# Performance work log

Measured on AMD Instinct MI355X. Metric: run time of the kernel, lower is better.

Reference implementation:

```python
import jax, jax.numpy as jnp
import numpy as np

D_MODEL = 2048
N_HEAD = 16
HEAD_DIM = D_MODEL // N_HEAD
FF_MULT = 4
LN_EPS = 1e-5


def layer_norm(x, w, b):
    mu = jnp.mean(x, axis=-1, keepdims=True)
    var = jnp.mean(jnp.square(x - mu), axis=-1, keepdims=True)
    return (x - mu) * jax.lax.rsqrt(var + LN_EPS) * w + b


def setup_inputs() -> dict:
    key = jax.random.key(0)
    ks = jax.random.split(key, 10)
    B, S, D = 2, 2048, D_MODEL
    s = 1.0 / np.sqrt(D)
    inp = {
        "x": jax.random.normal(ks[0], (B, S, D), jnp.float32),
        "token_emb": jax.random.normal(ks[1], (B, S, D), jnp.float32),
        # torch Linear weights are (out_features, in_features)
        "Wq": jax.random.normal(ks[2], (D, D), jnp.float32) * s,
        "Wk": jax.random.normal(ks[3], (D, D), jnp.float32) * s,
        "Wv": jax.random.normal(ks[4], (D, D), jnp.float32) * s,
        "Wo": jax.random.normal(ks[5], (D, D), jnp.float32) * s,
        "W1": jax.random.normal(ks[6], (FF_MULT * D, D), jnp.float32) * s,
        "W2": jax.random.normal(ks[7], (D, FF_MULT * D), jnp.float32) * (1.0 / np.sqrt(FF_MULT * D)),
        "ln1_w": jnp.ones((D,), jnp.float32),
        "ln1_b": jnp.zeros((D,), jnp.float32),
        "ln2_w": jnp.ones((D,), jnp.float32),
        "ln2_b": jnp.zeros((D,), jnp.float32),
    }
    return inp


def reference(x, token_emb, Wq, Wk, Wv, Wo, W1, W2, ln1_w, ln1_b, ln2_w, ln2_b):
    B, S, D = x.shape
    H, Hd = N_HEAD, HEAD_DIM

    h_norm = layer_norm(x, ln1_w, ln1_b)
    # torch Linear: y = x @ W.T
    q = (h_norm @ Wq.T).reshape(B, S, H, Hd).transpose(0, 2, 1, 3)  # (B,H,S,Hd)
    k = (h_norm @ Wk.T).reshape(B, S, H, Hd).transpose(0, 2, 1, 3)
    v = (token_emb @ Wv.T).reshape(B, S, H, Hd).transpose(0, 2, 1, 3)

    scores = jnp.einsum("bhqd,bhkd->bhqk", q, k) / np.sqrt(Hd)
    causal = jnp.tril(jnp.ones((S, S), bool))  # (S,S)
    scores = jnp.where(causal, scores, -jnp.inf)
    weights = jax.nn.softmax(scores, axis=-1)

    attn = jnp.einsum("bhqk,bhkd->bhqd", weights, v)
    attn = attn.transpose(0, 2, 1, 3).reshape(B, S, D)
    attn = attn @ Wo.T
    x = x + attn

    h_ffn = layer_norm(x, ln2_w, ln2_b)
    ffn = jax.nn.gelu(h_ffn @ W1.T, approximate=False) @ W2.T
    return x + ffn
```

## Files before the change

kernel.cpp:

```cpp
#include <hip/hip_runtime.h>
#include <hip/hip_bf16.h>
#include <math.h>

#define D_MODEL 2048
#define SEQ     2048
#define BATCH   2
#define NTOK    (BATCH*SEQ)
#define NHEAD   16
#define HDIM    128
#define FF      8192

typedef float  f32x4  __attribute__((ext_vector_type(4)));
typedef __bf16 bf16x8 __attribute__((ext_vector_type(8)));

__device__ __forceinline__ unsigned short f2bfbits(float f) {
    unsigned u = __builtin_bit_cast(unsigned, f);
    return (unsigned short)((u + 0x7fffu + ((u >> 16) & 1u)) >> 16);
}
__device__ __forceinline__ __bf16 f2bf(float f) {
    unsigned short h = f2bfbits(f);
    return __builtin_bit_cast(__bf16, h);
}

__device__ __forceinline__ void gld_lds16(const void* g, void* l) {
    __builtin_amdgcn_global_load_lds(
        (const __attribute__((address_space(1))) unsigned int*)g,
        (__attribute__((address_space(3))) unsigned int*)l, 16, 0, 0);
}

#define BAR()      __builtin_amdgcn_s_barrier()
#define LGKM(N)    asm volatile("s_waitcnt lgkmcnt(" #N ")" ::: "memory")
#define VMCNT(N)   asm volatile("s_waitcnt vmcnt(" #N ")" ::: "memory")
#define SCHEDB()   __builtin_amdgcn_sched_barrier(0)

__global__ __launch_bounds__(256) void cvt_all(
        const float* __restrict__ tok, const float* __restrict__ wq,
        const float* __restrict__ wk,  const float* __restrict__ wv,
        const float* __restrict__ wo,  const float* __restrict__ w1,
        const float* __restrict__ w2,
        __bf16* __restrict__ tokb, __bf16* __restrict__ wqb,
        __bf16* __restrict__ wkb,  __bf16* __restrict__ wvb,
        __bf16* __restrict__ wob,  __bf16* __restrict__ w1b,
        __bf16* __restrict__ w2b) {
    const size_t M4 = 4u * 1024 * 1024;
    size_t i = (size_t)blockIdx.x * 1024 + (size_t)threadIdx.x * 4;
    const float* src; __bf16* dst; size_t off;
    if      (i < 2*M4)  { src = tok; dst = tokb; off = i; }
    else if (i < 3*M4)  { src = wq;  dst = wqb;  off = i - 2*M4; }
    else if (i < 4*M4)  { src = wk;  dst = wkb;  off = i - 3*M4; }
    else if (i < 5*M4)  { src = wv;  dst = wvb;  off = i - 4*M4; }
    else if (i < 6*M4)  { src = wo;  dst = wob;  off = i - 5*M4; }
    else if (i < 10*M4) { src = w1;  dst = w1b;  off = i - 6*M4; }
    else                { src = w2;  dst = w2b;  off = i - 10*M4; }
    float4 v = *(const float4*)(src + off);
    ushort4 o;
    o.x = f2bfbits(v.x); o.y = f2bfbits(v.y);
    o.z = f2bfbits(v.z); o.w = f2bfbits(v.w);
    *(ushort4*)((unsigned short*)dst + off) = o;
}

__global__ __launch_bounds__(256) void add_reduce(
        const float* __restrict__ p0, const float* __restrict__ p1,
        const float* __restrict__ resid, float* __restrict__ out) {
    int i = blockIdx.x * 256 + threadIdx.x;
    float4 a = ((const float4*)p0)[i];
    float4 b = ((const float4*)p1)[i];
    float4 r = ((const float4*)resid)[i];
    float4 o;
    o.x = a.x + b.x + r.x; o.y = a.y + b.y + r.y;
    o.z = a.z + b.z + r.z; o.w = a.w + b.w + r.w;
    ((float4*)out)[i] = o;
}

__global__ __launch_bounds__(256) void ln_bf16(
        const float* __restrict__ x, const float* __restrict__ w,
        const float* __restrict__ b, __bf16* __restrict__ out) {
    const int row = blockIdx.x;
    const int tid = threadIdx.x;
    const float* xr = x + (size_t)row * D_MODEL;
    float4 v0 = *(const float4*)(xr + tid * 8);
    float4 v1 = *(const float4*)(xr + tid * 8 + 4);
    float va[8] = {v0.x, v0.y, v0.z, v0.w, v1.x, v1.y, v1.z, v1.w};
    float s = 0.f, ss = 0.f;
#pragma unroll
    for (int j = 0; j < 8; ++j) { s += va[j]; ss += va[j] * va[j]; }
#pragma unroll
    for (int m = 32; m; m >>= 1) { s += __shfl_xor(s, m, 64); ss += __shfl_xor(ss, m, 64); }
    __shared__ float red[8];
    const int wid = tid >> 6;
    if ((tid & 63) == 0) { red[wid * 2] = s; red[wid * 2 + 1] = ss; }
    __syncthreads();
    s  = red[0] + red[2] + red[4] + red[6];
    ss = red[1] + red[3] + red[5] + red[7];
    const float mu   = s * (1.0f / D_MODEL);
    const float var  = ss * (1.0f / D_MODEL) - mu * mu;
    const float rstd = rsqrtf(var + 1e-5f);
    const int c = tid * 8;
    ushort4 o0, o1;
    unsigned short ob[8];
#pragma unroll
    for (int j = 0; j < 8; ++j)
        ob[j] = f2bfbits((va[j] - mu) * rstd * w[c + j] + b[c + j]);
    o0.x = ob[0]; o0.y = ob[1]; o0.z = ob[2]; o0.w = ob[3];
    o1.x = ob[4]; o1.y = ob[5]; o1.z = ob[6]; o1.w = ob[7];
    ushort4* op = (ushort4*)(out + (size_t)row * D_MODEL + c);
    op[0] = o0; op[1] = o1;
}


template <int EPI, int MM>
__device__ __forceinline__ void gemm_epi(
        f32x4 (*acc)[4], int BMsz, int WMsz,
        int bm, int bn, int wm, int wn, int lhi, int l16,
        int M, int N, int slice,
        __bf16* __restrict__ Cb, float* __restrict__ Cf,
        const float* __restrict__ resid) {
#pragma unroll
    for (int m = 0; m < MM; ++m) {
        const int row = bm * BMsz + wm * WMsz + m * 16 + lhi * 4;
#pragma unroll
        for (int n = 0; n < 4; ++n) {
            const int col = bn * 256 + wn * 64 + n * 16 + l16;
            if (EPI == 3) {
                const int h = col >> 7, hd = col & 127;
                const size_t obase =
                    ((((size_t)(row >> 11) * NHEAD + h) * HDIM + hd) << 11) + (row & 2047);
                ushort4 o;
                o.x = f2bfbits(acc[m][n][0]); o.y = f2bfbits(acc[m][n][1]);
                o.z = f2bfbits(acc[m][n][2]); o.w = f2bfbits(acc[m][n][3]);
                *(ushort4*)((unsigned short*)Cb + obase) = o;
            } else {
#pragma unroll
                for (int r = 0; r < 4; ++r) {
                    float v = acc[m][n][r];
                    size_t off = (size_t)(row + r) * N + col;
                    if (EPI == 0) {
                        Cb[off] = f2bf(v);
                    } else if (EPI == 1) {
                        Cb[off] = f2bf(0.5f * v * (1.0f + erff(v * 0.70710678118654752f)));
                    } else if (EPI == 2) {
                        Cf[off] = v + resid[off];
                    } else {
                        Cf[(size_t)slice * M * N + off] = v;
                    }
                }
            }
        }
    }
}

template <int EPI, int SPLITK, int GEO>
__device__ __forceinline__ void gemm_core(
        const __bf16* __restrict__ A, const __bf16* __restrict__ Bm,
        __bf16* __restrict__ Cb, float* __restrict__ Cf,
        const float* __restrict__ resid, int M, int N, int K,
        int bm, int bn, int slice, char* smem) {
    const int tid = threadIdx.x;
    const int wid = tid >> 6, lane = tid & 63;
    const int l16 = lane & 15, lhi = lane >> 4;
    const int wm = wid >> 2, wn = wid & 3;
    const int tps = (K >> 6) / SPLITK;
    const int t0 = slice * tps, t1 = t0 + tps;

    const int trow = tid >> 3;
    const int XsT  = ((tid & 7) << 4) ^ ((trow & 7) << 4);
    const int dstT = tid * 16;
    const int maskL = (l16 & 7) << 4;
    const int colK0 = (lhi * 16) ^ maskL;
    const int colK1 = (64 + lhi * 16) ^ maskL;

    if constexpr (GEO == 0) {
        const __bf16* Ag = A  + (size_t)bm * 256 * K;
        const __bf16* Bg = Bm + (size_t)bn * 256 * K;
        const char* sA[4];
        const char* sB[4];
#pragma unroll
        for (int q = 0; q < 4; ++q) {
            sA[q] = (const char*)(Ag + (size_t)(trow + q * 64) * K) + XsT;
            sB[q] = (const char*)(Bg + (size_t)(trow + q * 64) * K) + XsT;
        }
        const int offA = (wm * 128 + l16) * 128;
        const int offB = 32768 + (wn * 64 + l16) * 128;

        f32x4 acc[8][4] = {};
        bf16x8 af0[4][2], af1[4][2], bq0[2][2], bq1[2][2];
        const char *pA0, *pA1, *pB0, *pB1;
        auto ldA = [&](bf16x8 (&dst)[4][2], int qm) {
#pragma unroll
            for (int i = 0; i < 4; ++i) {
                dst[i][0] = *(const bf16x8*)(pA0 + (qm * 4 + i) * 2048);
                dst[i][1] = *(const bf16x8*)(pA1 + (qm * 4 + i) * 2048);
            }
        };
        auto ldB = [&](bf16x8 (&dst)[2][2], int qn) {
#pragma unroll
            for (int j = 0; j < 2; ++j) {
                dst[j][0] = *(const bf16x8*)(pB0 + (qn * 2 + j) * 2048);
                dst[j][1] = *(const bf16x8*)(pB1 + (qn * 2 + j) * 2048);
            }
        };
        auto mfmaQ = [&](bf16x8 (&a)[4][2], bf16x8 (&b)[2][2], int mo, int no) {
#pragma unroll
            for (int i = 0; i < 4; ++i)
#pragma unroll
                for (int j = 0; j < 2; ++j)
#pragma unroll
                    for (int ks = 0; ks < 2; ++ks)
                        acc[mo + i][no + j] = __builtin_amdgcn_mfma_f32_16x16x32_bf16(
                            a[i][ks], b[j][ks], acc[mo + i][no + j], 0, 0, 0);
        };
        auto stageT = [&](int t, int c) {
            char* bA = smem + c * 65536;
            char* bB = bA + 32768;
            const size_t ko = (size_t)t * 128;
#pragma unroll
            for (int q = 0; q < 4; ++q)
                gld_lds16(sA[q] + ko, bA + q * 8192 + dstT);
#pragma unroll
            for (int q = 0; q < 4; ++q)
                gld_lds16(sB[q] + ko, bB + q * 8192 + dstT);
        };

        stageT(t0, 0);
        VMCNT(0);
        BAR();

        for (int t = t0; t < t1; ++t) {
            const int cur = (t - t0) & 1;
            const char* base = smem + cur * 65536;
            pA0 = base + offA + colK0;
            pA1 = base + offA + colK1;
            pB0 = base + offB + colK0;
            pB1 = base + offB + colK1;
            const bool pf = (t + 1 < t1);
            if (pf) stageT(t + 1, cur ^ 1);
            ldA(af0, 0); ldB(bq0, 0);
            __builtin_amdgcn_s_setprio(1);
            mfmaQ(af0, bq0, 0, 0);
            ldB(bq1, 1);
            mfmaQ(af0, bq1, 0, 2);
            ldA(af1, 1);
            mfmaQ(af1, bq0, 4, 0);
            mfmaQ(af1, bq1, 4, 2);
            __builtin_amdgcn_s_setprio(0);
            if (pf) VMCNT(0);
            BAR();
        }
        gemm_epi<EPI, 8>(acc, 256, 128, bm, bn, wm, wn, lhi, l16,
                         M, N, slice, Cb, Cf, resid);
    } else {
        const __bf16* Ag = A  + (size_t)bm * 128 * K;
        const __bf16* Bg = Bm + (size_t)bn * 256 * K;
        const char* sA[2];
        const char* sB[4];
#pragma unroll
        for (int q = 0; q < 2; ++q)
            sA[q] = (const char*)(Ag + (size_t)(trow + q * 64) * K) + XsT;
#pragma unroll
        for (int q = 0; q < 4; ++q)
            sB[q] = (const char*)(Bg + (size_t)(trow + q * 64) * K) + XsT;
        const int offA = (wm * 64 + l16) * 128;
        const int offB = 16384 + (wn * 64 + l16) * 128;

        f32x4 acc[4][4] = {};
        auto stageT = [&](int t, int c) {
            char* base = smem + c * 49152;
            const size_t ko = (size_t)t * 128;
#pragma unroll
            for (int q = 0; q < 2; ++q)
                gld_lds16(sA[q] + ko, base + q * 8192 + dstT);
#pragma unroll
            for (int q = 0; q < 4; ++q)
                gld_lds16(sB[q] + ko, base + 16384 + q * 8192 + dstT);
        };
        stageT(t0, 0);
        if (t0 + 1 < t1) {
            stageT(t0 + 1, 1);
            VMCNT(6);
        } else {
            VMCNT(0);
        }
        BAR();

        for (int t = t0; t < t1; ++t) {
            const int c = (t - t0) % 3;
            if (t + 2 < t1) stageT(t + 2, (c + 2) % 3);
            const char* base = smem + c * 49152;
            const char* pA0 = base + offA + colK0;
            const char* pA1 = base + offA + colK1;
            const char* pB0 = base + offB + colK0;
            const char* pB1 = base + offB + colK1;
            bf16x8 af[4][2], bq[4][2];
#pragma unroll
            for (int i = 0; i < 4; ++i) {
                af[i][0] = *(const bf16x8*)(pA0 + i * 2048);
                af[i][1] = *(const bf16x8*)(pA1 + i * 2048);
            }
#pragma unroll
            for (int j = 0; j < 4; ++j) {
                bq[j][0] = *(const bf16x8*)(pB0 + j * 2048);
                bq[j][1] = *(const bf16x8*)(pB1 + j * 2048);
            }
            __builtin_amdgcn_s_setprio(1);
#pragma unroll
            for (int i = 0; i < 4; ++i)
#pragma unroll
                for (int j = 0; j < 4; ++j)
#pragma unroll
                    for (int ks = 0; ks < 2; ++ks)
                        acc[i][j] = __builtin_amdgcn_mfma_f32_16x16x32_bf16(
                            af[i][ks], bq[j][ks], acc[i][j], 0, 0, 0);
            __builtin_amdgcn_s_setprio(0);
            if (t + 2 < t1) {
                VMCNT(6);
                BAR();
            } else if (t + 1 < t1) {
                VMCNT(0);
                BAR();
            }
        }
        gemm_epi<EPI, 4>(acc, 128, 64, bm, bn, wm, wn, lhi, l16,
                         M, N, slice, Cb, Cf, resid);
    }
}

template <int EPI, int SPLITK, int GEO, int MAP>
__global__ __launch_bounds__(512, 2) void gemm_k(
        const __bf16* __restrict__ A, const __bf16* __restrict__ Bm,
        __bf16* __restrict__ Cb, float* __restrict__ Cf,
        const float* __restrict__ resid, int M, int N, int K) {
    __shared__ __align__(16) char smem[GEO ? 147456 : 131072];
    int bm, bn, slice = 0;
    if (MAP == 0) {
        int id = blockIdx.x;
        const int cpx = gridDim.x >> 3;
        id = (id & 7) * cpx + (id >> 3);
        const int nbn = N >> 8;
        if (SPLITK == 2) {
            const int nblk = (M >> (GEO ? 7 : 8)) * nbn;
            slice = id / nblk;
            id -= slice * nblk;
        }
        bm = id / nbn; bn = id % nbn;
    } else if (MAP == 1) {
        const int x = blockIdx.x & 7, j = blockIdx.x >> 3;
        bn = (x << 2) | (j & 3); bm = j >> 2;
    } else {
        const int x = blockIdx.x & 7, j = blockIdx.x >> 3;
        bm = (x << 2) | (j & 3); bn = j >> 2;
    }
    gemm_core<EPI, SPLITK, GEO>(A, Bm, Cb, Cf, resid, M, N, K, bm, bn, slice, smem);
}

__global__ __launch_bounds__(512, 2) void gemm_qkv(
        const __bf16* __restrict__ hn, const __bf16* __restrict__ wqk,
        __bf16* __restrict__ QKb, const __bf16* __restrict__ tokb,
        const __bf16* __restrict__ wv, __bf16* __restrict__ Vtg) {
    __shared__ __align__(16) char smem[147456];
    const int x = blockIdx.x & 7, j = blockIdx.x >> 3;
    if (j < 32) {
        const int bm = ((x >> 1) << 2) | (j & 3);
        const int bn = ((x & 1) << 3) | (j >> 2);
        gemm_core<0, 1, 0>(hn, wqk, QKb, nullptr, nullptr,
                           NTOK, 2 * D_MODEL, D_MODEL, bm, bn, 0, smem);
    } else {
        const int jv = j - 32;
        const int bm = ((x >> 1) << 3) | (jv & 7);
        const int bn = ((x & 1) << 2) | (jv >> 3);
        gemm_core<3, 1, 1>(tokb, wv, Vtg, nullptr, nullptr,
                           NTOK, D_MODEL, D_MODEL, bm, bn, 0, smem);
    }
}

#define LDQK 4096
__global__ __launch_bounds__(512) void attn_causal(
        const __bf16* __restrict__ Q, const __bf16* __restrict__ K,
        const __bf16* __restrict__ Vt, __bf16* __restrict__ O) {
    const int qt = gridDim.x - 1 - blockIdx.x;
    const int h = blockIdx.y, bb = blockIdx.z;
    const int tid = threadIdx.x, wid = tid >> 6, lane = tid & 63;
    const int l16 = lane & 15, lhi = lane >> 4;
    __shared__ __align__(16) __bf16 Ks[2][64 * 128];
    __shared__ __align__(16) __bf16 Vs[128 * 64];
    __shared__ __align__(16) __bf16 Pl[8][16 * 72];

    const size_t qkbase = ((size_t)bb * SEQ) * LDQK + (size_t)h * HDIM;
    const size_t obase  = ((size_t)bb * SEQ) * D_MODEL + (size_t)h * HDIM;
    const size_t vtbase = (((size_t)bb * NHEAD + h) * HDIM) << 11;
    const int q0 = qt * 128 + wid * 16;

    bf16x8 qf[4];
#pragma unroll
    for (int ks = 0; ks < 4; ++ks)
        qf[ks] = *(const bf16x8*)(Q + qkbase + (size_t)(q0 + l16) * LDQK + ks * 32 + lhi * 8);

    auto stageK = [&](int kt, int buf) {
#pragma unroll
        for (int j = 0; j < 2; ++j) {
            int idx = j * 512 + tid;
            int row = idx >> 4, c8 = idx & 15;
            int c8s = c8 ^ (row & 7);
            gld_lds16(K + qkbase + (size_t)(kt * 64 + row) * LDQK + c8s * 8,
                      &Ks[buf][0] + idx * 8);
        }
    };
    auto stageV = [&](int kt) {
#pragma unroll
        for (int j = 0; j < 2; ++j) {
            int idx = j * 512 + tid;
            int row = idx >> 3, c8 = idx & 7;
            int c8s = c8 ^ (row & 7);
            gld_lds16(Vt + vtbase + (size_t)row * SEQ + kt * 64 + c8s * 8, Vs + idx * 8);
        }
    };

    f32x4 accO[8] = {};
    float m_run[4], l_run[4];
#pragma unroll
    for (int r = 0; r < 4; ++r) { m_run[r] = -1e30f; l_run[r] = 0.f; }

    const float scale2 = 0.08838834764831845f * 1.4426950408889634f;
    const int NKT = (qt + 1) * 2;

    stageK(0, 0);
    VMCNT(0);
    BAR();
    SCHEDB();

    for (int kt = 0; kt < NKT; ++kt) {
        const int cb = kt & 1;
        const bool pf = (kt + 1 < NKT);
        stageV(kt);
        if (pf) stageK(kt + 1, cb ^ 1);

        f32x4 s[4] = {};
        __builtin_amdgcn_s_setprio(1);
#pragma unroll
        for (int nb = 0; nb < 4; ++nb) {
            const int tok = nb * 16 + l16;
#pragma unroll
            for (int ks = 0; ks < 4; ++ks) {
                int co = (ks * 64 + lhi * 16) ^ ((tok & 7) << 4);
                bf16x8 kf = *(const bf16x8*)((const char*)&Ks[cb][0] + tok * 256 + co);
                s[nb] = __builtin_amdgcn_mfma_f32_16x16x32_bf16(qf[ks], kf, s[nb], 0, 0, 0);
            }
        }
        __builtin_amdgcn_s_setprio(0);

        if (((kt + 1) << 6) > q0) {
#pragma unroll
            for (int nb = 0; nb < 4; ++nb)
#pragma unroll
                for (int r = 0; r < 4; ++r) {
                    float sv = s[nb][r] * scale2;
                    if ((kt * 64 + nb * 16 + l16) > (q0 + lhi * 4 + r)) sv = -1e30f;
                    s[nb][r] = sv;
                }
        } else {
#pragma unroll
            for (int nb = 0; nb < 4; ++nb)
#pragma unroll
                for (int r = 0; r < 4; ++r) s[nb][r] *= scale2;
        }

        float alpha[4];
#pragma unroll
        for (int r = 0; r < 4; ++r) {
            float mx = fmaxf(fmaxf(s[0][r], s[1][r]), fmaxf(s[2][r], s[3][r]));
#pragma unroll
            for (int m = 8; m; m >>= 1) mx = fmaxf(mx, __shfl_xor(mx, m, 64));
            float mnew = fmaxf(m_run[r], mx);
            alpha[r] = exp2f(m_run[r] - mnew);
            float rs = 0.f;
#pragma unroll
            for (int nb = 0; nb < 4; ++nb) {
                float p = exp2f(s[nb][r] - mnew);
                s[nb][r] = p;
                rs += p;
            }
#pragma unroll
            for (int m = 8; m; m >>= 1) rs += __shfl_xor(rs, m, 64);
            l_run[r] = l_run[r] * alpha[r] + rs;
            m_run[r] = mnew;
        }
#pragma unroll
        for (int d8 = 0; d8 < 8; ++d8)
#pragma unroll
            for (int r = 0; r < 4; ++r) accO[d8][r] *= alpha[r];
#pragma unroll
        for (int nb = 0; nb < 4; ++nb)
#pragma unroll
            for (int r = 0; r < 4; ++r)
                Pl[wid][(lhi * 4 + r) * 72 + nb * 16 + l16] = f2bf(s[nb][r]);

        if (pf) { VMCNT(2); } else { VMCNT(0); }
        BAR();
        SCHEDB();

        __builtin_amdgcn_s_setprio(1);
#pragma unroll
        for (int ks2 = 0; ks2 < 2; ++ks2) {
            bf16x8 pa = *(const bf16x8*)(&Pl[wid][l16 * 72 + ks2 * 32 + lhi * 8]);
#pragma unroll
            for (int d8 = 0; d8 < 8; ++d8) {
                const int d = d8 * 16 + l16;
                const int co = ((ks2 * 4 + lhi) ^ (d & 7)) << 4;
                bf16x8 vf = *(const bf16x8*)((const char*)Vs + d * 128 + co);
                accO[d8] = __builtin_amdgcn_mfma_f32_16x16x32_bf16(pa, vf, accO[d8], 0, 0, 0);
            }
        }
        __builtin_amdgcn_s_setprio(0);

        VMCNT(0);
        BAR();
        SCHEDB();
    }

#pragma unroll
    for (int d8 = 0; d8 < 8; ++d8)
#pragma unroll
        for (int r = 0; r < 4; ++r) {
            float o = accO[d8][r] / l_run[r];
            O[obase + (size_t)(q0 + lhi * 4 + r) * D_MODEL + d8 * 16 + l16] = f2bf(o);
        }
}

extern "C" void kernel_launch(void* const* d_in, const int* in_sizes, int n_in,
                              void* d_out, int out_size, void* d_ws, size_t ws_size,
                              hipStream_t stream) {
    const float* x    = (const float*)d_in[0];
    const float* tok  = (const float*)d_in[1];
    const float* Wq   = (const float*)d_in[2];
    const float* Wk   = (const float*)d_in[3];
    const float* Wv   = (const float*)d_in[4];
    const float* Wo   = (const float*)d_in[5];
    const float* W1   = (const float*)d_in[6];
    const float* W2   = (const float*)d_in[7];
    const float* ln1w = (const float*)d_in[8];
    const float* ln1b = (const float*)d_in[9];
    const float* ln2w = (const float*)d_in[10];
    const float* ln2b = (const float*)d_in[11];
    float* out = (float*)d_out;

    char* ws = (char*)d_ws;
    size_t off = 0;
    auto alloc = [&](size_t bytes) { void* p = ws + off; off += bytes; return p; };
    __bf16* tokb  = (__bf16*)alloc((size_t)NTOK * D_MODEL * 2);
    __bf16* hnorm = (__bf16*)alloc((size_t)NTOK * D_MODEL * 2);
    __bf16* wqb   = (__bf16*)alloc((size_t)D_MODEL * D_MODEL * 2);
    __bf16* wkb   = (__bf16*)alloc((size_t)D_MODEL * D_MODEL * 2);
    __bf16* wvb   = (__bf16*)alloc((size_t)D_MODEL * D_MODEL * 2);
    __bf16* wob   = (__bf16*)alloc((size_t)D_MODEL * D_MODEL * 2);
    __bf16* w1b   = (__bf16*)alloc((size_t)FF * D_MODEL * 2);
    __bf16* w2b   = (__bf16*)alloc((size_t)D_MODEL * FF * 2);
    __bf16* QKb   = (__bf16*)alloc((size_t)NTOK * 2 * D_MODEL * 2);
    __bf16* Vtg   = (__bf16*)alloc((size_t)NTOK * D_MODEL * 2);
    __bf16* Ab    = (__bf16*)alloc((size_t)NTOK * D_MODEL * 2);
    float*  x2    = (float*)alloc((size_t)NTOK * D_MODEL * 4);
    __bf16* gb    = QKb;
    float*  p0    = (float*)(ws);
    float*  p1    = p0 + (size_t)NTOK * D_MODEL;

    cvt_all<<<56 * 1024, 256, 0, stream>>>(tok, Wq, Wk, Wv, Wo, W1, W2,
                                           tokb, wqb, wkb, wvb, wob, w1b, w2b);

    ln_bf16<<<NTOK, 256, 0, stream>>>(x, ln1w, ln1b, hnorm);

    gemm_qkv<<<512, 512, 0, stream>>>(hnorm, wqb, QKb, tokb, wvb, Vtg);

    attn_causal<<<dim3(SEQ / 128, NHEAD, BATCH), 512, 0, stream>>>(QKb, QKb + D_MODEL, Vtg, Ab);

    gemm_k<2, 1, 1, 2><<<256, 512, 0, stream>>>(Ab, wob, nullptr, x2, x,
                                                NTOK, D_MODEL, D_MODEL);

    ln_bf16<<<NTOK, 256, 0, stream>>>(x2, ln2w, ln2b, hnorm);

    gemm_k<1, 1, 0, 1><<<512, 512, 0, stream>>>(hnorm, w1b, gb, nullptr, nullptr,
                                                NTOK, FF, D_MODEL);
    gemm_k<4, 2, 0, 0><<<256, 512, 0, stream>>>(gb, w2b, nullptr, p0, nullptr,
                                                NTOK, D_MODEL, FF);
    add_reduce<<<(NTOK * D_MODEL) / 1024, 256, 0, stream>>>(p0, p1, x2, out);
}
```

Before: 633.3 us.

## Fuse LN1 into conversion kernel, lazy softmax rescale, fold residual into split-K

Merges the first layernorm into the weight and activation bf16 conversion kernel, removing one launch. In attention, the online softmax skips the rescale of the running max and accumulator when the row max grows by at most 8 (log2 units), avoiding exp and multiply work on most tiles. The split-K FFN2 GEMM now writes slice 0 plus the residual straight to the output and slice 1 to a scratch buffer, so the final reduce reads two arrays instead of three. The lazy rescale adds a wave-wide vote and a branch, and lets probabilities reach up to 2^8 before bf16 conversion.

New measurement: 686.8 us. 8.4% more time.

```diff
diff --git a/kernel.cpp b/kernel.cpp
--- a/kernel.cpp
+++ b/kernel.cpp
@@ -33,7 +33,9 @@
 #define VMCNT(N)   asm volatile("s_waitcnt vmcnt(" #N ")" ::: "memory")
 #define SCHEDB()   __builtin_amdgcn_sched_barrier(0)
 
-__global__ __launch_bounds__(256) void cvt_all(
+__global__ __launch_bounds__(256) void prep(
+        const float* __restrict__ x, const float* __restrict__ ln1w,
+        const float* __restrict__ ln1b, __bf16* __restrict__ hnorm,
         const float* __restrict__ tok, const float* __restrict__ wq,
         const float* __restrict__ wk,  const float* __restrict__ wv,
         const float* __restrict__ wo,  const float* __restrict__ w1,
@@ -42,34 +44,63 @@
         __bf16* __restrict__ wkb,  __bf16* __restrict__ wvb,
         __bf16* __restrict__ wob,  __bf16* __restrict__ w1b,
         __bf16* __restrict__ w2b) {
-    const size_t M4 = 4u * 1024 * 1024;
-    size_t i = (size_t)blockIdx.x * 1024 + (size_t)threadIdx.x * 4;
-    const float* src; __bf16* dst; size_t off;
-    if      (i < 2*M4)  { src = tok; dst = tokb; off = i; }
-    else if (i < 3*M4)  { src = wq;  dst = wqb;  off = i - 2*M4; }
-    else if (i < 4*M4)  { src = wk;  dst = wkb;  off = i - 3*M4; }
-    else if (i < 5*M4)  { src = wv;  dst = wvb;  off = i - 4*M4; }
-    else if (i < 6*M4)  { src = wo;  dst = wob;  off = i - 5*M4; }
-    else if (i < 10*M4) { src = w1;  dst = w1b;  off = i - 6*M4; }
-    else                { src = w2;  dst = w2b;  off = i - 10*M4; }
-    float4 v = *(const float4*)(src + off);
-    ushort4 o;
-    o.x = f2bfbits(v.x); o.y = f2bfbits(v.y);
-    o.z = f2bfbits(v.z); o.w = f2bfbits(v.w);
-    *(ushort4*)((unsigned short*)dst + off) = o;
-}
-
-__global__ __launch_bounds__(256) void add_reduce(
-        const float* __restrict__ p0, const float* __restrict__ p1,
-        const float* __restrict__ resid, float* __restrict__ out) {
+    const int tid = threadIdx.x;
+    if (blockIdx.x < NTOK) {
+        const int row = blockIdx.x;
+        const float* xr = x + (size_t)row * D_MODEL;
+        float4 v0 = *(const float4*)(xr + tid * 8);
+        float4 v1 = *(const float4*)(xr + tid * 8 + 4);
+        float va[8] = {v0.x, v0.y, v0.z, v0.w, v1.x, v1.y, v1.z, v1.w};
+        float s = 0.f, ss = 0.f;
+#pragma unroll
+        for (int j = 0; j < 8; ++j) { s += va[j]; ss += va[j] * va[j]; }
+#pragma unroll
+        for (int m = 32; m; m >>= 1) { s += __shfl_xor(s, m, 64); ss += __shfl_xor(ss, m, 64); }
+        __shared__ float red[8];
+        const int wid = tid >> 6;
+        if ((tid & 63) == 0) { red[wid * 2] = s; red[wid * 2 + 1] = ss; }
+        __syncthreads();
+        s  = red[0] + red[2] + red[4] + red[6];
+        ss = red[1] + red[3] + red[5] + red[7];
+        const float mu   = s * (1.0f / D_MODEL);
+        const float var  = ss * (1.0f / D_MODEL) - mu * mu;
+        const float rstd = rsqrtf(var + 1e-5f);
+        const int c = tid * 8;
+        ushort4 o0, o1;
+        unsigned short ob[8];
+#pragma unroll
+        for (int j = 0; j < 8; ++j)
+            ob[j] = f2bfbits((va[j] - mu) * rstd * ln1w[c + j] + ln1b[c + j]);
+        o0.x = ob[0]; o0.y = ob[1]; o0.z = ob[2]; o0.w = ob[3];
+        o1.x = ob[4]; o1.y = ob[5]; o1.z = ob[6]; o1.w = ob[7];
+        ushort4* op = (ushort4*)(hnorm + (size_t)row * D_MODEL + c);
+        op[0] = o0; op[1] = o1;
+    } else {
+        const size_t M4 = 4u * 1024 * 1024;
+        size_t i = (size_t)(blockIdx.x - NTOK) * 1024 + (size_t)tid * 4;
+        const float* src; __bf16* dst; size_t off;
+        if      (i < 2*M4)  { src = tok; dst = tokb; off = i; }
+        else if (i < 3*M4)  { src = wq;  dst = wqb;  off = i - 2*M4; }
+        else if (i < 4*M4)  { src = wk;  dst = wkb;  off = i - 3*M4; }
+        else if (i < 5*M4)  { src = wv;  dst = wvb;  off = i - 4*M4; }
+        else if (i < 6*M4)  { src = wo;  dst = wob;  off = i - 5*M4; }
+        else if (i < 10*M4) { src = w1;  dst = w1b;  off = i - 6*M4; }
+        else                { src = w2;  dst = w2b;  off = i - 10*M4; }
+        float4 v = *(const float4*)(src + off);
+        ushort4 o;
+        o.x = f2bfbits(v.x); o.y = f2bfbits(v.y);
+        o.z = f2bfbits(v.z); o.w = f2bfbits(v.w);
+        *(ushort4*)((unsigned short*)dst + off) = o;
+    }
+}
+
+__global__ __launch_bounds__(256) void add_reduce2(
+        const float* __restrict__ p1, float* __restrict__ out) {
     int i = blockIdx.x * 256 + threadIdx.x;
-    float4 a = ((const float4*)p0)[i];
+    float4 a = ((const float4*)out)[i];
     float4 b = ((const float4*)p1)[i];
-    float4 r = ((const float4*)resid)[i];
-    float4 o;
-    o.x = a.x + b.x + r.x; o.y = a.y + b.y + r.y;
-    o.z = a.z + b.z + r.z; o.w = a.w + b.w + r.w;
-    ((float4*)out)[i] = o;
+    a.x += b.x; a.y += b.y; a.z += b.z; a.w += b.w;
+    ((float4*)out)[i] = a;
 }
 
 __global__ __launch_bounds__(256) void ln_bf16(
@@ -140,8 +171,11 @@
                         Cb[off] = f2bf(0.5f * v * (1.0f + erff(v * 0.70710678118654752f)));
                     } else if (EPI == 2) {
                         Cf[off] = v + resid[off];
+                    } else if (EPI == 4) {
+                        Cf[(size_t)slice * M * N + off] = v;
                     } else {
-                        Cf[(size_t)slice * M * N + off] = v;
+                        if (slice == 0) Cf[off] = v + resid[off];
+                        else            ((float*)Cb)[off] = v;
                     }
                 }
             }
@@ -463,30 +497,50 @@
                 for (int r = 0; r < 4; ++r) s[nb][r] *= scale2;
         }
 
-        float alpha[4];
+        float mx[4];
 #pragma unroll
         for (int r = 0; r < 4; ++r) {
-            float mx = fmaxf(fmaxf(s[0][r], s[1][r]), fmaxf(s[2][r], s[3][r]));
-#pragma unroll
-            for (int m = 8; m; m >>= 1) mx = fmaxf(mx, __shfl_xor(mx, m, 64));
-            float mnew = fmaxf(m_run[r], mx);
-            alpha[r] = exp2f(m_run[r] - mnew);
-            float rs = 0.f;
-#pragma unroll
-            for (int nb = 0; nb < 4; ++nb) {
-                float p = exp2f(s[nb][r] - mnew);
-                s[nb][r] = p;
-                rs += p;
-            }
-#pragma unroll
-            for (int m = 8; m; m >>= 1) rs += __shfl_xor(rs, m, 64);
-            l_run[r] = l_run[r] * alpha[r] + rs;
-            m_run[r] = mnew;
-        }
-#pragma unroll
-        for (int d8 = 0; d8 < 8; ++d8)
-#pragma unroll
-            for (int r = 0; r < 4; ++r) accO[d8][r] *= alpha[r];
+            float m0 = fmaxf(fmaxf(s[0][r], s[1][r]), fmaxf(s[2][r], s[3][r]));
+#pragma unroll
+            for (int m = 8; m; m >>= 1) m0 = fmaxf(m0, __shfl_xor(m0, m, 64));
+            mx[r] = m0;
+        }
+        const float dd = fmaxf(fmaxf(mx[0] - m_run[0], mx[1] - m_run[1]),
+                               fmaxf(mx[2] - m_run[2], mx[3] - m_run[3]));
+        if (__all(dd <= 8.0f)) {
+#pragma unroll
+            for (int r = 0; r < 4; ++r) {
+                float rs = 0.f;
+#pragma unroll
+                for (int nb = 0; nb < 4; ++nb) {
+                    float p = exp2f(s[nb][r] - m_run[r]);
+                    s[nb][r] = p;
+                    rs += p;
+                }
+#pragma unroll
+                for (int m = 8; m; m >>= 1) rs += __shfl_xor(rs, m, 64);
+                l_run[r] += rs;
+            }
+        } else {
+#pragma unroll
+            for (int r = 0; r < 4; ++r) {
+                float mnew = fmaxf(m_run[r], mx[r]);
+                float al = exp2f(m_run[r] - mnew);
+                float rs = 0.f;
+#pragma unroll
+                for (int nb = 0; nb < 4; ++nb) {
+                    float p = exp2f(s[nb][r] - mnew);
+                    s[nb][r] = p;
+                    rs += p;
+                }
+#pragma unroll
+                for (int m = 8; m; m >>= 1) rs += __shfl_xor(rs, m, 64);
+                l_run[r] = l_run[r] * al + rs;
+                m_run[r] = mnew;
+#pragma unroll
+                for (int d8 = 0; d8 < 8; ++d8) accO[d8][r] *= al;
+            }
+        }
 #pragma unroll
         for (int nb = 0; nb < 4; ++nb)
 #pragma unroll
@@ -558,13 +612,12 @@
     __bf16* Ab    = (__bf16*)alloc((size_t)NTOK * D_MODEL * 2);
     float*  x2    = (float*)alloc((size_t)NTOK * D_MODEL * 4);
     __bf16* gb    = QKb;
-    float*  p0    = (float*)(ws);
-    float*  p1    = p0 + (size_t)NTOK * D_MODEL;
-
-    cvt_all<<<56 * 1024, 256, 0, stream>>>(tok, Wq, Wk, Wv, Wo, W1, W2,
-                                           tokb, wqb, wkb, wvb, wob, w1b, w2b);
-
-    ln_bf16<<<NTOK, 256, 0, stream>>>(x, ln1w, ln1b, hnorm);
+    float*  p1    = (float*)ws;
+
+    prep<<<NTOK + 56 * 1024, 256, 0, stream>>>(
+        x, ln1w, ln1b, hnorm,
+        tok, Wq, Wk, Wv, Wo, W1, W2,
+        tokb, wqb, wkb, wvb, wob, w1b, w2b);
 
     gemm_qkv<<<512, 512, 0, stream>>>(hnorm, wqb, QKb, tokb, wvb, Vtg);
 
@@ -577,7 +630,7 @@
 
     gemm_k<1, 1, 0, 1><<<512, 512, 0, stream>>>(hnorm, w1b, gb, nullptr, nullptr,
                                                 NTOK, FF, D_MODEL);
-    gemm_k<4, 2, 0, 0><<<256, 512, 0, stream>>>(gb, w2b, nullptr, p0, nullptr,
+    gemm_k<5, 2, 0, 0><<<256, 512, 0, stream>>>(gb, w2b, (__bf16*)p1, out, x2,
                                                 NTOK, D_MODEL, FF);
-    add_reduce<<<(NTOK * D_MODEL) / 1024, 256, 0, stream>>>(p0, p1, x2, out);
-}
+    add_reduce2<<<(NTOK * D_MODEL) / 1024, 256, 0, stream>>>(p1, out);
+}
```
